# Performance work log

Measured on AMD Instinct MI355X. Metric: run time of the kernel, lower is better.

The kernel has to match this reference:

```python
import jax, jax.numpy as jnp
import numpy as np
import math

D_MODEL = 1024
HEADS = 16
HEAD_DIM = D_MODEL // HEADS
BATCH = 2
SEQ = 2048


def setup_inputs() -> dict:
    key = jax.random.key(0)
    ks = jax.random.split(key, 6)
    scale = 1.0 / math.sqrt(D_MODEL)
    return {
        "x": jax.random.normal(ks[0], (BATCH, SEQ, D_MODEL), dtype=jnp.float32),
        "mask": jnp.zeros((SEQ, SEQ), dtype=jnp.float32),
        "w_qkv": jax.random.normal(ks[1], (D_MODEL, 3 * D_MODEL), dtype=jnp.float32) * scale,
        "b_qkv": jax.random.normal(ks[2], (3 * D_MODEL,), dtype=jnp.float32) * 0.01,
        "w_out": jax.random.normal(ks[3], (D_MODEL, D_MODEL), dtype=jnp.float32) * scale,
        "b_out": jax.random.normal(ks[4], (D_MODEL,), dtype=jnp.float32) * 0.01,
    }


def reference(x, mask, w_qkv, b_qkv, w_out, b_out):
    B, S, D = x.shape
    H, hd = HEADS, HEAD_DIM
    # fused QKV projection: [B,S,3D]
    qkv = x @ w_qkv + b_qkv
    # [B,S,H,3*hd] -> [B,H,S,3*hd]
    qkv = qkv.reshape(B, S, H, 3 * hd).transpose(0, 2, 1, 3)
    q, k, v = jnp.split(qkv, 3, axis=-1)  # each [B,H,S,hd]
    inv_sqrt_d = jnp.asarray(1.0 / math.sqrt(hd), dtype=x.dtype)
    scores = jnp.einsum("bhqd,bhkd->bhqk", q, k) * inv_sqrt_d
    # additive mask; [S,S] broadcasts identically in [H,B,S,S] or [B,H,S,S] layout
    scores = scores + mask
    attn = jax.nn.softmax(scores, axis=-1)
    vals = jnp.einsum("bhqk,bhkd->bhqd", attn, v)  # [B,H,S,hd]
    vals = vals.transpose(0, 2, 1, 3).reshape(B, S, H * hd)
    return vals @ w_out + b_out
```

## Files before the change

### kernel.cpp

```cpp
#include <hip/hip_runtime.h>


typedef __bf16 bf16;
typedef __bf16 bf16x2 __attribute__((ext_vector_type(2)));
typedef __bf16 bf16x4 __attribute__((ext_vector_type(4)));
typedef __bf16 bf16x8 __attribute__((ext_vector_type(8)));
typedef float f32x4 __attribute__((ext_vector_type(4)));
typedef float f32x16 __attribute__((ext_vector_type(16)));

#define MFMA(a, b, c) __builtin_amdgcn_mfma_f32_16x16x32_bf16((a), (b), (c), 0, 0, 0)
#define MFMA32(a, b, c) __builtin_amdgcn_mfma_f32_32x32x16_bf16((a), (b), (c), 0, 0, 0)

#if __has_builtin(__builtin_amdgcn_exp2f)
#define EXP2(x) __builtin_amdgcn_exp2f(x)
#else
#define EXP2(x) exp2f(x)
#endif

__device__ __forceinline__ void load_lds16(const bf16* g, void* l) {
    __builtin_amdgcn_global_load_lds(
        (const __attribute__((address_space(1))) unsigned int*)g,
        (__attribute__((address_space(3))) unsigned int*)l, 16, 0, 0);
}

__global__ void cast4_kernel(const float* __restrict__ in, bf16* __restrict__ out, int n4) {
    int i = blockIdx.x * blockDim.x + threadIdx.x;
    if (i < n4) {
        float4 v = ((const float4*)in)[i];
        bf16x4 o = {(bf16)v.x, (bf16)v.y, (bf16)v.z, (bf16)v.w};
        ((bf16x4*)out)[i] = o;
    }
}

__global__ void transpose_cast_kernel(const float* __restrict__ in, bf16* __restrict__ out,
                                      int R, int C) {
    __shared__ float tile[32][33];
    int bx = blockIdx.x * 32;
    int by = blockIdx.y * 32;
    int tx = threadIdx.x, ty = threadIdx.y;
    for (int i = 0; i < 32; i += 8)
        tile[ty + i][tx] = in[(size_t)(by + ty + i) * C + bx + tx];
    __syncthreads();
    for (int i = 0; i < 32; i += 8)
        out[(size_t)(bx + ty + i) * R + by + tx] = (bf16)tile[tx][ty + i];
}

__global__ __launch_bounds__(256) void gemm_qkv_kernel(
    const bf16* __restrict__ A, const bf16* __restrict__ BT,
    const float* __restrict__ bias,
    bf16* __restrict__ Q, bf16* __restrict__ K, bf16* __restrict__ VT) {
    __shared__ __attribute__((aligned(16))) char lds[2][16384];
    int bm = blockIdx.x, bn = blockIdx.y;
    int t = threadIdx.x;
    int w = t >> 6, lane = t & 63, g = lane >> 4, l16 = lane & 15;
    int wm = (w >> 1) * 64, wn = (w & 1) * 64;
    f32x4 acc[4][4] = {};
    const bf16* Ablk = A + (size_t)(bm * 128) * 1024;
    const bf16* Bblk = BT + (size_t)(bn * 128) * 1024;
    int srow = t >> 2;
    int scg = (t & 3) ^ (srow & 3);
    const bf16* ag0 = Ablk + (size_t)srow * 1024 + scg * 8;
    const bf16* ag1 = ag0 + 64 * 1024;
    const bf16* bg0 = Bblk + (size_t)srow * 1024 + scg * 8;
    const bf16* bg1 = bg0 + 64 * 1024;

    load_lds16(ag0, lds[0] + t * 16);
    load_lds16(ag1, lds[0] + 4096 + t * 16);
    load_lds16(bg0, lds[0] + 8192 + t * 16);
    load_lds16(bg1, lds[0] + 12288 + t * 16);
    asm volatile("s_waitcnt vmcnt(0)" ::: "memory");

    int sw = l16 & 3;
#pragma unroll 2
    for (int j = 0; j < 32; j++) {
        asm volatile("s_barrier" ::: "memory");
        int jp = j + 1 < 32 ? j + 1 : 31;
        char* dst = lds[(j + 1) & 1];
        load_lds16(ag0 + jp * 32, dst + t * 16);
        load_lds16(ag1 + jp * 32, dst + 4096 + t * 16);
        load_lds16(bg0 + jp * 32, dst + 8192 + t * 16);
        load_lds16(bg1 + jp * 32, dst + 12288 + t * 16);

        const bf16* As = (const bf16*)lds[j & 1];
        const bf16* Bs = (const bf16*)(lds[j & 1] + 8192);
        bf16x8 af[4], bfr[4];
#pragma unroll
        for (int mi = 0; mi < 4; mi++) {
            int row = wm + mi * 16 + l16;
            af[mi] = *(const bf16x8*)(&As[row * 32 + (g ^ sw) * 8]);
        }
#pragma unroll
        for (int ni = 0; ni < 4; ni++) {
            int row = wn + ni * 16 + l16;
            bfr[ni] = *(const bf16x8*)(&Bs[row * 32 + (g ^ sw) * 8]);
        }
#pragma unroll
        for (int mi = 0; mi < 4; mi++)
#pragma unroll
            for (int ni = 0; ni < 4; ni++)
                acc[mi][ni] = MFMA(bfr[ni], af[mi], acc[mi][ni]);
        asm volatile("s_waitcnt vmcnt(0)" ::: "memory");
    }
    __syncthreads();

    bf16* vt = (bf16*)lds;
    int b = bm >> 4;
    int row0 = (bm & 15) * 128 + wm;
    int half_col = bn * 128 + wn;
    int h = half_col / 192, tt = half_col % 192;
    size_t bh = (size_t)(b * 16 + h);

    if (tt < 128) {
        bf16* base = (tt == 0 ? Q : K) + bh * 2048 * 64;
#pragma unroll
        for (int mi = 0; mi < 4; mi++) {
#pragma unroll
            for (int ni = 0; ni < 4; ni++) {
                int d0 = ni * 16 + g * 4;
                float4 bv = *(const float4*)(&bias[half_col + d0]);
                int s = row0 + mi * 16 + l16;
                bf16x4 pk = {(bf16)(acc[mi][ni][0] + bv.x), (bf16)(acc[mi][ni][1] + bv.y),
                             (bf16)(acc[mi][ni][2] + bv.z), (bf16)(acc[mi][ni][3] + bv.w)};
                *(bf16x4*)(&base[(size_t)s * 64 + d0]) = pk;
            }
        }
    } else {
#pragma unroll
        for (int mi = 0; mi < 4; mi++) {
            int s_local = wm + mi * 16 + l16;
#pragma unroll
            for (int ni = 0; ni < 4; ni++) {
                int d0 = ni * 16 + g * 4;
                float4 bv = *(const float4*)(&bias[half_col + d0]);
                vt[(d0 + 0) * 136 + s_local] = (bf16)(acc[mi][ni][0] + bv.x);
                vt[(d0 + 1) * 136 + s_local] = (bf16)(acc[mi][ni][1] + bv.y);
                vt[(d0 + 2) * 136 + s_local] = (bf16)(acc[mi][ni][2] + bv.z);
                vt[(d0 + 3) * 136 + s_local] = (bf16)(acc[mi][ni][3] + bv.w);
            }
        }
    }
    __syncthreads();

    int hc0 = bn * 128, hc1 = bn * 128 + 64;
    int vhalf = (hc0 % 192 == 128) ? 0 : ((hc1 % 192 == 128) ? 1 : -1);
    if (vhalf >= 0) {
        int vcol = bn * 128 + vhalf * 64;
        size_t vbh = (size_t)(b * 16 + vcol / 192);
        int d = t >> 2, ch = t & 3;
        const bf16* src = &vt[d * 136 + ch * 32];
        bf16* dstp = &VT[(vbh * 64 + d) * 2048 + (bm & 15) * 128 + ch * 32];
#pragma unroll
        for (int k = 0; k < 4; k++)
            *(bf16x8*)(&dstp[k * 8]) = *(const bf16x8*)(&src[k * 8]);
    }
}

__global__ __launch_bounds__(256) void gemm_out_kernel(
    const bf16* __restrict__ A, const bf16* __restrict__ BT,
    const float* __restrict__ bias, float* __restrict__ out) {
    __shared__ __attribute__((aligned(16))) char lds[2][12288];
    int bm = blockIdx.x, bn = blockIdx.y;
    int t = threadIdx.x;
    int w = t >> 6, lane = t & 63, g = lane >> 4, l16 = lane & 15;
    int wm = (w >> 1) * 64, wn = (w & 1) * 32;
    f32x4 acc[4][2] = {};
    const bf16* Ablk = A + (size_t)(bm * 128) * 1024;
    const bf16* Bblk = BT + (size_t)(bn * 64) * 1024;
    int srow = t >> 2;
    int scg = (t & 3) ^ (srow & 3);
    const bf16* ag0 = Ablk + (size_t)srow * 1024 + scg * 8;
    const bf16* ag1 = ag0 + 64 * 1024;
    const bf16* bg0 = Bblk + (size_t)srow * 1024 + scg * 8;

    load_lds16(ag0, lds[0] + t * 16);
    load_lds16(ag1, lds[0] + 4096 + t * 16);
    load_lds16(bg0, lds[0] + 8192 + t * 16);
    asm volatile("s_waitcnt vmcnt(0)" ::: "memory");

    int sw = l16 & 3;
#pragma unroll 2
    for (int j = 0; j < 32; j++) {
        asm volatile("s_barrier" ::: "memory");
        int jp = j + 1 < 32 ? j + 1 : 31;
        char* dst = lds[(j + 1) & 1];
        load_lds16(ag0 + jp * 32, dst + t * 16);
        load_lds16(ag1 + jp * 32, dst + 4096 + t * 16);
        load_lds16(bg0 + jp * 32, dst + 8192 + t * 16);

        const bf16* As = (const bf16*)lds[j & 1];
        const bf16* Bs = (const bf16*)(lds[j & 1] + 8192);
        bf16x8 af[4], bfr[2];
#pragma unroll
        for (int mi = 0; mi < 4; mi++) {
            int row = wm + mi * 16 + l16;
            af[mi] = *(const bf16x8*)(&As[row * 32 + (g ^ sw) * 8]);
        }
#pragma unroll
        for (int ni = 0; ni < 2; ni++) {
            int row = wn + ni * 16 + l16;
            bfr[ni] = *(const bf16x8*)(&Bs[row * 32 + (g ^ sw) * 8]);
        }
#pragma unroll
        for (int mi = 0; mi < 4; mi++)
#pragma unroll
            for (int ni = 0; ni < 2; ni++)
                acc[mi][ni] = MFMA(bfr[ni], af[mi], acc[mi][ni]);
        asm volatile("s_waitcnt vmcnt(0)" ::: "memory");
    }

#pragma unroll
    for (int mi = 0; mi < 4; mi++) {
#pragma unroll
        for (int ni = 0; ni < 2; ni++) {
            int row = bm * 128 + wm + mi * 16 + l16;
            int col0 = bn * 64 + wn + ni * 16 + g * 4;
            float4 bv = *(const float4*)(&bias[col0]);
            float4 ov = {acc[mi][ni][0] + bv.x, acc[mi][ni][1] + bv.y,
                         acc[mi][ni][2] + bv.z, acc[mi][ni][3] + bv.w};
            *(float4*)(&out[(size_t)row * 1024 + col0]) = ov;
        }
    }
}

__global__ __launch_bounds__(256, 2) void attn_kernel(
    const bf16* __restrict__ Q, const bf16* __restrict__ K,
    const bf16* __restrict__ VT, const float* __restrict__ mask,
    bf16* __restrict__ vals) {
    __shared__ __attribute__((aligned(16))) char lds[4][8192];

    int blk = blockIdx.x;
    int bh = ((blk & 7) << 2) | ((blk >> 3) & 3);
    int qt = blk >> 5;
    int t = threadIdx.x;
    int w = t >> 6, lane = t & 63;
    int l32 = lane & 31, hi = lane >> 5;
    int qw = qt * 128 + w * 32;

    const bf16* Qp = Q + (size_t)bh * 2048 * 64;
    const bf16* Kp = K + (size_t)bh * 2048 * 64;
    const bf16* Vp = VT + (size_t)bh * 64 * 2048;
    const float* mrow = mask + (size_t)(qw + l32) * 2048;

    int ks_row = t >> 3;
    int ks_cblk = (t & 7) ^ (ks_row & 7);
    const bf16* kg = Kp + ks_row * 64 + ks_cblk * 8;
    int vs_d = t >> 2;
    int vs_sblk = (t & 3) ^ ((t >> 3) & 3);
    const bf16* vg = Vp + (size_t)vs_d * 2048 + vs_sblk * 8;

    const float SCL = 0.125f * 1.44269504089f;
    const float L2E = 1.44269504089f;

    bf16x8 qf[4];
#pragma unroll
    for (int t4 = 0; t4 < 4; t4++)
        qf[t4] = *(const bf16x8*)(&Qp[(size_t)(qw + l32) * 64 + t4 * 16 + hi * 8]);

    load_lds16(kg + 0, lds[0] + t * 16);
    load_lds16(vg + 0, lds[0] + 4096 + t * 16);
    float4 mc0 = *(const float4*)(&mrow[0 + hi * 4]);
    float4 mc1 = *(const float4*)(&mrow[8 + hi * 4]);
    float4 mc2 = *(const float4*)(&mrow[16 + hi * 4]);
    float4 mc3 = *(const float4*)(&mrow[24 + hi * 4]);
    load_lds16(kg + 32 * 64, lds[1] + t * 16);
    load_lds16(vg + 32, lds[1] + 4096 + t * 16);
    asm volatile("s_waitcnt vmcnt(0)" ::: "memory");
    asm volatile("s_barrier" ::: "memory");

    f32x16 o0 = {}, o1 = {};
    const f32x16 kZero = {};
    float la = 0.f;

    union { unsigned u[4]; bf16x8 v; } pp0, pp1;
    pp0.u[0] = 0; pp0.u[1] = 0; pp0.u[2] = 0; pp0.u[3] = 0;
    pp1.u[0] = 0; pp1.u[1] = 0; pp1.u[2] = 0; pp1.u[3] = 0;
    bf16x8 vfp0 = {}, vfp1 = {}, vfp2 = {}, vfp3 = {};

    int slot0 = (l32 * 8 + ((2 * 0 + hi) ^ (l32 & 7))) * 16;
    int slot1 = (l32 * 8 + ((2 * 1 + hi) ^ (l32 & 7))) * 16;
    int slot2 = (l32 * 8 + ((2 * 2 + hi) ^ (l32 & 7))) * 16;
    int slot3 = (l32 * 8 + ((2 * 3 + hi) ^ (l32 & 7))) * 16;
    int d0l = l32, d1l = 32 + l32;
    int sv00 = 4096 + (d0l * 4 + ((2 * 0 + hi) ^ ((d0l >> 1) & 3))) * 16;
    int sv01 = 4096 + (d0l * 4 + ((2 * 1 + hi) ^ ((d0l >> 1) & 3))) * 16;
    int sv10 = 4096 + (d1l * 4 + ((2 * 0 + hi) ^ ((d1l >> 1) & 3))) * 16;
    int sv11 = 4096 + (d1l * 4 + ((2 * 1 + hi) ^ ((d1l >> 1) & 3))) * 16;
    bool hib = hi != 0;

    for (int j = 0; j < 64; j++) {
        const char* bufp = lds[j & 3];
        int jm = j + 1 < 64 ? j + 1 : 63;
        float4 nm0 = *(const float4*)(&mrow[jm * 32 + 0 + hi * 4]);
        float4 nm1 = *(const float4*)(&mrow[jm * 32 + 8 + hi * 4]);
        float4 nm2 = *(const float4*)(&mrow[jm * 32 + 16 + hi * 4]);
        float4 nm3 = *(const float4*)(&mrow[jm * 32 + 24 + hi * 4]);
        int jp = j + 2 < 64 ? j + 2 : 63;
        char* dstp = lds[(j + 2) & 3];
        load_lds16(kg + (size_t)jp * 32 * 64, dstp + t * 16);
        load_lds16(vg + jp * 32, dstp + 4096 + t * 16);
        asm volatile("s_waitcnt vmcnt(12)" ::: "memory");
        asm volatile("s_barrier" ::: "memory");

        bf16x8 kf0 = *(const bf16x8*)(&bufp[slot0]);
        bf16x8 kf1 = *(const bf16x8*)(&bufp[slot1]);
        bf16x8 kf2 = *(const bf16x8*)(&bufp[slot2]);
        bf16x8 kf3 = *(const bf16x8*)(&bufp[slot3]);

        o0 = MFMA32(vfp0, pp0.v, o0);
        o0 = MFMA32(vfp1, pp1.v, o0);
        o1 = MFMA32(vfp2, pp0.v, o1);
        o1 = MFMA32(vfp3, pp1.v, o1);

        f32x16 s;
        s = MFMA32(kf0, qf[0], kZero);
        s = MFMA32(kf1, qf[1], s);
        s = MFMA32(kf2, qf[2], s);
        s = MFMA32(kf3, qf[3], s);

        float p[16];
        p[0]  = EXP2(s[0] * SCL + mc0.x * L2E);
        p[1]  = EXP2(s[1] * SCL + mc0.y * L2E);
        p[2]  = EXP2(s[2] * SCL + mc0.z * L2E);
        p[3]  = EXP2(s[3] * SCL + mc0.w * L2E);
        p[4]  = EXP2(s[4] * SCL + mc1.x * L2E);
        p[5]  = EXP2(s[5] * SCL + mc1.y * L2E);
        p[6]  = EXP2(s[6] * SCL + mc1.z * L2E);
        p[7]  = EXP2(s[7] * SCL + mc1.w * L2E);
        p[8]  = EXP2(s[8] * SCL + mc2.x * L2E);
        p[9]  = EXP2(s[9] * SCL + mc2.y * L2E);
        p[10] = EXP2(s[10] * SCL + mc2.z * L2E);
        p[11] = EXP2(s[11] * SCL + mc2.w * L2E);
        p[12] = EXP2(s[12] * SCL + mc3.x * L2E);
        p[13] = EXP2(s[13] * SCL + mc3.y * L2E);
        p[14] = EXP2(s[14] * SCL + mc3.z * L2E);
        p[15] = EXP2(s[15] * SCL + mc3.w * L2E);
        {
            float a0 = p[0] + p[1], a1 = p[2] + p[3], a2 = p[4] + p[5], a3 = p[6] + p[7];
            float a4 = p[8] + p[9], a5 = p[10] + p[11], a6 = p[12] + p[13], a7 = p[14] + p[15];
            float b0 = a0 + a1, b1 = a2 + a3, b2 = a4 + a5, b3 = a6 + a7;
            la += (b0 + b1) + (b2 + b3);
        }

        unsigned dw0, dw1, dw2, dw3, dw4, dw5, dw6, dw7;
        {
            union { bf16x2 h; unsigned u; } u;
            u.h = bf16x2{(bf16)p[0],  (bf16)p[1]};  dw0 = u.u;
            u.h = bf16x2{(bf16)p[2],  (bf16)p[3]};  dw1 = u.u;
            u.h = bf16x2{(bf16)p[4],  (bf16)p[5]};  dw2 = u.u;
            u.h = bf16x2{(bf16)p[6],  (bf16)p[7]};  dw3 = u.u;
            u.h = bf16x2{(bf16)p[8],  (bf16)p[9]};  dw4 = u.u;
            u.h = bf16x2{(bf16)p[10], (bf16)p[11]}; dw5 = u.u;
            u.h = bf16x2{(bf16)p[12], (bf16)p[13]}; dw6 = u.u;
            u.h = bf16x2{(bf16)p[14], (bf16)p[15]}; dw7 = u.u;
        }
        unsigned r0 = (unsigned)__shfl_xor((int)(hib ? dw0 : dw2), 32, 64);
        unsigned r1 = (unsigned)__shfl_xor((int)(hib ? dw1 : dw3), 32, 64);
        unsigned r2 = (unsigned)__shfl_xor((int)(hib ? dw4 : dw6), 32, 64);
        unsigned r3 = (unsigned)__shfl_xor((int)(hib ? dw5 : dw7), 32, 64);
        pp0.u[0] = hib ? r0 : dw0;
        pp0.u[1] = hib ? r1 : dw1;
        pp0.u[2] = hib ? dw2 : r0;
        pp0.u[3] = hib ? dw3 : r1;
        pp1.u[0] = hib ? r2 : dw4;
        pp1.u[1] = hib ? r3 : dw5;
        pp1.u[2] = hib ? dw6 : r2;
        pp1.u[3] = hib ? dw7 : r3;

        vfp0 = *(const bf16x8*)(&bufp[sv00]);
        vfp1 = *(const bf16x8*)(&bufp[sv01]);
        vfp2 = *(const bf16x8*)(&bufp[sv10]);
        vfp3 = *(const bf16x8*)(&bufp[sv11]);

        mc0 = nm0; mc1 = nm1; mc2 = nm2; mc3 = nm3;
    }
    o0 = MFMA32(vfp0, pp0.v, o0);
    o0 = MFMA32(vfp1, pp1.v, o0);
    o1 = MFMA32(vfp2, pp0.v, o1);
    o1 = MFMA32(vfp3, pp1.v, o1);
    asm volatile("s_waitcnt vmcnt(0)" ::: "memory");

    la += __shfl_xor(la, 32, 64);
    int b = bh >> 4, hh = bh & 15;
    float li = 1.f / la;
    size_t row = (size_t)(b * 2048 + qw + l32);
#pragma unroll
    for (int rg = 0; rg < 4; rg++) {
        bf16x4 pk0 = {(bf16)(o0[rg * 4 + 0] * li), (bf16)(o0[rg * 4 + 1] * li),
                      (bf16)(o0[rg * 4 + 2] * li), (bf16)(o0[rg * 4 + 3] * li)};
        *(bf16x4*)(&vals[row * 1024 + hh * 64 + rg * 8 + hi * 4]) = pk0;
        bf16x4 pk1 = {(bf16)(o1[rg * 4 + 0] * li), (bf16)(o1[rg * 4 + 1] * li),
                      (bf16)(o1[rg * 4 + 2] * li), (bf16)(o1[rg * 4 + 3] * li)};
        *(bf16x4*)(&vals[row * 1024 + hh * 64 + 32 + rg * 8 + hi * 4]) = pk1;
    }
}

extern "C" void kernel_launch(void* const* d_in, const int* in_sizes, int n_in,
                              void* d_out, int out_size, void* d_ws, size_t ws_size,
                              hipStream_t stream) {
    const float* x     = (const float*)d_in[0];
    const float* mask  = (const float*)d_in[1];
    const float* w_qkv = (const float*)d_in[2];
    const float* b_qkv = (const float*)d_in[3];
    const float* w_out = (const float*)d_in[4];
    const float* b_out = (const float*)d_in[5];
    float* out = (float*)d_out;

    char* ws = (char*)d_ws;
    size_t off = 0;
    bf16* xb    = (bf16*)(ws + off); off += (size_t)4096 * 1024 * 2;
    bf16* wqkvT = (bf16*)(ws + off); off += (size_t)3072 * 1024 * 2;
    bf16* woutT = (bf16*)(ws + off); off += (size_t)1024 * 1024 * 2;
    bf16* Qa    = (bf16*)(ws + off); off += (size_t)32 * 2048 * 64 * 2;
    bf16* Ka    = (bf16*)(ws + off); off += (size_t)32 * 2048 * 64 * 2;
    bf16* VTa   = (bf16*)(ws + off); off += (size_t)32 * 64 * 2048 * 2;
    bf16* vals  = (bf16*)(ws + off); off += (size_t)4096 * 1024 * 2;

    cast4_kernel<<<4096, 256, 0, stream>>>(x, xb, 4096 * 1024 / 4);
    transpose_cast_kernel<<<dim3(96, 32), dim3(32, 8), 0, stream>>>(w_qkv, wqkvT, 1024, 3072);
    transpose_cast_kernel<<<dim3(32, 32), dim3(32, 8), 0, stream>>>(w_out, woutT, 1024, 1024);
    gemm_qkv_kernel<<<dim3(32, 24), 256, 0, stream>>>(xb, wqkvT, b_qkv, Qa, Ka, VTa);
    attn_kernel<<<512, 256, 0, stream>>>(Qa, Ka, VTa, mask, vals);
    gemm_out_kernel<<<dim3(32, 16), 256, 0, stream>>>(vals, woutT, b_out, out);
}
```

Baseline: 231.9 us.

## Fuse prep kernels and pre-convert mask to permuted bf16 scaled by log2e

Merges the x cast and the two weight transpose-casts into one prep kernel launch, which also converts the fp32 mask into bf16 pre-multiplied by log2(e). The bf16 mask is permuted so each lane reads its 16 values with two 16-byte loads instead of four float4 loads. This halves mask traffic in the attention loop and removes a multiply per score, which is why the vmcnt wait threshold is adjusted. In exchange it adds a full mask conversion pass and rounds the mask to bf16, which could change results for non-trivial masks.

```diff
diff --git a/kernel.cpp b/kernel.cpp
--- a/kernel.cpp
+++ b/kernel.cpp
@@ -23,26 +23,50 @@
         (__attribute__((address_space(3))) unsigned int*)l, 16, 0, 0);
 }
 
-__global__ void cast4_kernel(const float* __restrict__ in, bf16* __restrict__ out, int n4) {
-    int i = blockIdx.x * blockDim.x + threadIdx.x;
-    if (i < n4) {
-        float4 v = ((const float4*)in)[i];
+__global__ __launch_bounds__(256) void prep_kernel(
+    const float* __restrict__ x, bf16* __restrict__ xb,
+    const float* __restrict__ w_qkv, bf16* __restrict__ wqkvT,
+    const float* __restrict__ w_out, bf16* __restrict__ woutT,
+    const float* __restrict__ mask, bf16* __restrict__ maskb) {
+    __shared__ float tile[32][33];
+    int blk = blockIdx.x;
+    int t = threadIdx.x;
+    if (blk < 4096) {
+        int i = blk * 256 + t;
+        float4 v = ((const float4*)x)[i];
         bf16x4 o = {(bf16)v.x, (bf16)v.y, (bf16)v.z, (bf16)v.w};
-        ((bf16x4*)out)[i] = o;
-    }
-}
-
-__global__ void transpose_cast_kernel(const float* __restrict__ in, bf16* __restrict__ out,
-                                      int R, int C) {
-    __shared__ float tile[32][33];
-    int bx = blockIdx.x * 32;
-    int by = blockIdx.y * 32;
-    int tx = threadIdx.x, ty = threadIdx.y;
-    for (int i = 0; i < 32; i += 8)
-        tile[ty + i][tx] = in[(size_t)(by + ty + i) * C + bx + tx];
-    __syncthreads();
-    for (int i = 0; i < 32; i += 8)
-        out[(size_t)(bx + ty + i) * R + by + tx] = (bf16)tile[tx][ty + i];
+        ((bf16x4*)xb)[i] = o;
+    } else if (blk < 4096 + 3072) {
+        int flat = blk - 4096;
+        int bx = (flat % 96) * 32, by = (flat / 96) * 32;
+        int tx = t & 31, ty = t >> 5;
+        for (int i = 0; i < 32; i += 8)
+            tile[ty + i][tx] = w_qkv[(size_t)(by + ty + i) * 3072 + bx + tx];
+        __syncthreads();
+        for (int i = 0; i < 32; i += 8)
+            wqkvT[(size_t)(bx + ty + i) * 1024 + by + tx] = (bf16)tile[tx][ty + i];
+    } else if (blk < 4096 + 3072 + 1024) {
+        int flat = blk - (4096 + 3072);
+        int bx = (flat % 32) * 32, by = (flat / 32) * 32;
+        int tx = t & 31, ty = t >> 5;
+        for (int i = 0; i < 32; i += 8)
+            tile[ty + i][tx] = w_out[(size_t)(by + ty + i) * 1024 + bx + tx];
+        __syncthreads();
+        for (int i = 0; i < 32; i += 8)
+            woutT[(size_t)(bx + ty + i) * 1024 + by + tx] = (bf16)tile[tx][ty + i];
+    } else {
+        int flat = blk - (4096 + 3072 + 1024);
+        int idx4 = flat * 256 + t;
+        float4 v = ((const float4*)mask)[idx4];
+        int row = idx4 >> 9;
+        int k = (idx4 & 511) * 4;
+        int g = (k & 31) >> 2;
+        int pos = (k & ~31) + ((g & 1) << 4) + ((g >> 1) << 2);
+        const float L2E = 1.44269504089f;
+        bf16x4 o = {(bf16)(v.x * L2E), (bf16)(v.y * L2E),
+                    (bf16)(v.z * L2E), (bf16)(v.w * L2E)};
+        *(bf16x4*)(&maskb[(size_t)row * 2048 + pos]) = o;
+    }
 }
 
 __global__ __launch_bounds__(256) void gemm_qkv_kernel(
@@ -224,7 +248,7 @@
 
 __global__ __launch_bounds__(256, 2) void attn_kernel(
     const bf16* __restrict__ Q, const bf16* __restrict__ K,
-    const bf16* __restrict__ VT, const float* __restrict__ mask,
+    const bf16* __restrict__ VT, const bf16* __restrict__ maskb,
     bf16* __restrict__ vals) {
     __shared__ __attribute__((aligned(16))) char lds[4][8192];
 
@@ -239,7 +263,7 @@
     const bf16* Qp = Q + (size_t)bh * 2048 * 64;
     const bf16* Kp = K + (size_t)bh * 2048 * 64;
     const bf16* Vp = VT + (size_t)bh * 64 * 2048;
-    const float* mrow = mask + (size_t)(qw + l32) * 2048;
+    const bf16* mrowb = maskb + (size_t)(qw + l32) * 2048 + hi * 16;
 
     int ks_row = t >> 3;
     int ks_cblk = (t & 7) ^ (ks_row & 7);
@@ -249,7 +273,6 @@
     const bf16* vg = Vp + (size_t)vs_d * 2048 + vs_sblk * 8;
 
     const float SCL = 0.125f * 1.44269504089f;
-    const float L2E = 1.44269504089f;
 
     bf16x8 qf[4];
 #pragma unroll
@@ -258,10 +281,8 @@
 
     load_lds16(kg + 0, lds[0] + t * 16);
     load_lds16(vg + 0, lds[0] + 4096 + t * 16);
-    float4 mc0 = *(const float4*)(&mrow[0 + hi * 4]);
-    float4 mc1 = *(const float4*)(&mrow[8 + hi * 4]);
-    float4 mc2 = *(const float4*)(&mrow[16 + hi * 4]);
-    float4 mc3 = *(const float4*)(&mrow[24 + hi * 4]);
+    bf16x8 mb0 = *(const bf16x8*)(&mrowb[0]);
+    bf16x8 mb1 = *(const bf16x8*)(&mrowb[8]);
     load_lds16(kg + 32 * 64, lds[1] + t * 16);
     load_lds16(vg + 32, lds[1] + 4096 + t * 16);
     asm volatile("s_waitcnt vmcnt(0)" ::: "memory");
@@ -290,15 +311,13 @@
     for (int j = 0; j < 64; j++) {
         const char* bufp = lds[j & 3];
         int jm = j + 1 < 64 ? j + 1 : 63;
-        float4 nm0 = *(const float4*)(&mrow[jm * 32 + 0 + hi * 4]);
-        float4 nm1 = *(const float4*)(&mrow[jm * 32 + 8 + hi * 4]);
-        float4 nm2 = *(const float4*)(&mrow[jm * 32 + 16 + hi * 4]);
-        float4 nm3 = *(const float4*)(&mrow[jm * 32 + 24 + hi * 4]);
+        bf16x8 nmb0 = *(const bf16x8*)(&mrowb[jm * 32]);
+        bf16x8 nmb1 = *(const bf16x8*)(&mrowb[jm * 32 + 8]);
         int jp = j + 2 < 64 ? j + 2 : 63;
         char* dstp = lds[(j + 2) & 3];
         load_lds16(kg + (size_t)jp * 32 * 64, dstp + t * 16);
         load_lds16(vg + jp * 32, dstp + 4096 + t * 16);
-        asm volatile("s_waitcnt vmcnt(12)" ::: "memory");
+        asm volatile("s_waitcnt vmcnt(8)" ::: "memory");
         asm volatile("s_barrier" ::: "memory");
 
         bf16x8 kf0 = *(const bf16x8*)(&bufp[slot0]);
@@ -318,22 +337,22 @@
         s = MFMA32(kf3, qf[3], s);
 
         float p[16];
-        p[0]  = EXP2(s[0] * SCL + mc0.x * L2E);
-        p[1]  = EXP2(s[1] * SCL + mc0.y * L2E);
-        p[2]  = EXP2(s[2] * SCL + mc0.z * L2E);
-        p[3]  = EXP2(s[3] * SCL + mc0.w * L2E);
-        p[4]  = EXP2(s[4] * SCL + mc1.x * L2E);
-        p[5]  = EXP2(s[5] * SCL + mc1.y * L2E);
-        p[6]  = EXP2(s[6] * SCL + mc1.z * L2E);
-        p[7]  = EXP2(s[7] * SCL + mc1.w * L2E);
-        p[8]  = EXP2(s[8] * SCL + mc2.x * L2E);
-        p[9]  = EXP2(s[9] * SCL + mc2.y * L2E);
-        p[10] = EXP2(s[10] * SCL + mc2.z * L2E);
-        p[11] = EXP2(s[11] * SCL + mc2.w * L2E);
-        p[12] = EXP2(s[12] * SCL + mc3.x * L2E);
-        p[13] = EXP2(s[13] * SCL + mc3.y * L2E);
-        p[14] = EXP2(s[14] * SCL + mc3.z * L2E);
-        p[15] = EXP2(s[15] * SCL + mc3.w * L2E);
+        p[0]  = EXP2(s[0]  * SCL + (float)mb0[0]);
+        p[1]  = EXP2(s[1]  * SCL + (float)mb0[1]);
+        p[2]  = EXP2(s[2]  * SCL + (float)mb0[2]);
+        p[3]  = EXP2(s[3]  * SCL + (float)mb0[3]);
+        p[4]  = EXP2(s[4]  * SCL + (float)mb0[4]);
+        p[5]  = EXP2(s[5]  * SCL + (float)mb0[5]);
+        p[6]  = EXP2(s[6]  * SCL + (float)mb0[6]);
+        p[7]  = EXP2(s[7]  * SCL + (float)mb0[7]);
+        p[8]  = EXP2(s[8]  * SCL + (float)mb1[0]);
+        p[9]  = EXP2(s[9]  * SCL + (float)mb1[1]);
+        p[10] = EXP2(s[10] * SCL + (float)mb1[2]);
+        p[11] = EXP2(s[11] * SCL + (float)mb1[3]);
+        p[12] = EXP2(s[12] * SCL + (float)mb1[4]);
+        p[13] = EXP2(s[13] * SCL + (float)mb1[5]);
+        p[14] = EXP2(s[14] * SCL + (float)mb1[6]);
+        p[15] = EXP2(s[15] * SCL + (float)mb1[7]);
         {
             float a0 = p[0] + p[1], a1 = p[2] + p[3], a2 = p[4] + p[5], a3 = p[6] + p[7];
             float a4 = p[8] + p[9], a5 = p[10] + p[11], a6 = p[12] + p[13], a7 = p[14] + p[15];
@@ -371,7 +390,7 @@
         vfp2 = *(const bf16x8*)(&bufp[sv10]);
         vfp3 = *(const bf16x8*)(&bufp[sv11]);
 
-        mc0 = nm0; mc1 = nm1; mc2 = nm2; mc3 = nm3;
+        mb0 = nmb0; mb1 = nmb1;
     }
     o0 = MFMA32(vfp0, pp0.v, o0);
     o0 = MFMA32(vfp1, pp1.v, o0);
@@ -414,11 +433,10 @@
     bf16* Ka    = (bf16*)(ws + off); off += (size_t)32 * 2048 * 64 * 2;
     bf16* VTa   = (bf16*)(ws + off); off += (size_t)32 * 64 * 2048 * 2;
     bf16* vals  = (bf16*)(ws + off); off += (size_t)4096 * 1024 * 2;
-
-    cast4_kernel<<<4096, 256, 0, stream>>>(x, xb, 4096 * 1024 / 4);
-    transpose_cast_kernel<<<dim3(96, 32), dim3(32, 8), 0, stream>>>(w_qkv, wqkvT, 1024, 3072);
-    transpose_cast_kernel<<<dim3(32, 32), dim3(32, 8), 0, stream>>>(w_out, woutT, 1024, 1024);
+    bf16* maskb = (bf16*)(ws + off); off += (size_t)2048 * 2048 * 2;
+
+    prep_kernel<<<12288, 256, 0, stream>>>(x, xb, w_qkv, wqkvT, w_out, woutT, mask, maskb);
     gemm_qkv_kernel<<<dim3(32, 24), 256, 0, stream>>>(xb, wqkvT, b_qkv, Qa, Ka, VTa);
-    attn_kernel<<<512, 256, 0, stream>>>(Qa, Ka, VTa, mask, vals);
+    attn_kernel<<<512, 256, 0, stream>>>(Qa, Ka, VTa, maskb, vals);
     gemm_out_kernel<<<dim3(32, 16), 256, 0, stream>>>(vals, woutT, b_out, out);
 }
```

Result: faster. 209.0 us (-9.9%).
